# Performance work log

Hardware: AMD Instinct MI355X
Metric: run time of the kernel (lower is better)

## Reference

```python
import jax, jax.numpy as jnp
import numpy as np

N_CHR = 23
N_EMB = 512
E_DIM = 128
B = 4
L = 2048


def setup_inputs() -> dict:
    key = jax.random.key(0)
    k1, k2, k3 = jax.random.split(key, 3)
    chromosome = jax.random.randint(k1, (B, N_CHR, L), 0, N_CHR)
    position = jax.random.uniform(k2, (B, N_CHR, L), dtype=jnp.float32)
    embeddings = jax.random.normal(k3, (N_CHR, N_EMB, E_DIM), dtype=jnp.float32)
    centers = jnp.tile(jnp.linspace(0.0, 1.0, N_EMB, dtype=jnp.float32)[None, :], (N_CHR, 1))  # [23,512]
    log_variances = jnp.full((N_CHR, N_EMB), -5.0, dtype=jnp.float32)
    return {
        "chromosome": chromosome,
        "position": position,
        "embeddings": embeddings,
        "centers": centers,
        "log_variances": log_variances,
    }


def reference(chromosome, position, embeddings, centers, log_variances):
    # position: [B, C=23, L]; centers/log_variances: [C, K=512]; embeddings: [C, K, E]
    variances = jnp.exp(log_variances)                       # [C, K]
    d = position[..., None] - centers[None, :, None, :]      # [B, C, L, K]
    rbf = jnp.exp(-(d * d) / (2.0 * variances[None, :, None, :]))
    weights = jax.nn.softmax(rbf, axis=-1)                   # softmax over codebook (matches torch)
    out = jnp.einsum("bclk,cke->bcle", weights, embeddings)  # [B, C, L, E]
    bsz = position.shape[0]
    return out.reshape(bsz, -1, embeddings.shape[-1])        # [B, C*L, E]
```

## Files before the change

kernel.cpp:

```cpp
#include <hip/hip_runtime.h>
#include <hip/hip_bf16.h>

#define N_CHR 23
#define N_EMB 512
#define E_DIM 128
#define B_SZ  4
#define L_SEQ 2048
#define LOG2E 1.4426950408889634f
#define LOG2_LOG2E 0.5287663729448977f

typedef __attribute__((ext_vector_type(8))) short short8;
typedef __attribute__((ext_vector_type(4))) float floatx4;
typedef __attribute__((ext_vector_type(2))) float f32x2;

#if __has_builtin(__builtin_amdgcn_exp2f)
#define EXP2(x) __builtin_amdgcn_exp2f(x)
#else
#define EXP2(x) __expf((x) * 0.6931471805599453f)
#endif

#if __has_builtin(__builtin_amdgcn_rcpf)
#define RCP(x) __builtin_amdgcn_rcpf(x)
#else
#define RCP(x) (1.0f / (x))
#endif

__device__ __forceinline__ float bf2f(unsigned short u) {
    return __uint_as_float(((unsigned)u) << 16);
}
__device__ __forceinline__ unsigned short f2bf(float f) {
    unsigned u = __float_as_uint(f);
    unsigned r = u + 0x7FFFu + ((u >> 16) & 1u);
    return (unsigned short)(r >> 16);
}

__global__ __launch_bounds__(256) void emb_pack_kernel(
    const float* __restrict__ emb, uint4* __restrict__ embw)
{
    const int idx  = blockIdx.x * 256 + threadIdx.x;
    const int lane = idx & 63;
    const int nt   = (idx >> 6) & 7;
    const int ch   = (idx >> 9) & 15;
    const int c    = idx >> 13;
    if (c >= N_CHR) return;
    const int quad = lane >> 4;
    const int n    = nt * 16 + (lane & 15);
    const float* src = emb + (size_t)(c * N_EMB + ch * 32 + quad * 8) * E_DIM + n;
    unsigned v[8];
#pragma unroll
    for (int j = 0; j < 8; ++j) v[j] = (unsigned)f2bf(src[j * E_DIM]);
    uint4 w;
    w.x = v[0] | (v[1] << 16);
    w.y = v[2] | (v[3] << 16);
    w.z = v[4] | (v[5] << 16);
    w.w = v[6] | (v[7] << 16);
    embw[idx] = w;
}

__global__ __launch_bounds__(256, 7) void rbf_emb_kernel(
    const float* __restrict__ pos,
    const uint4* __restrict__ embw,
    const float* __restrict__ ctr,
    const float* __restrict__ lvar,
    float* __restrict__ out)
{
    __shared__ float2 cs_s[N_EMB];
    __shared__ uint4 Bs[2][512];

    const int tid  = threadIdx.x;
    const int lane = tid & 63;
    const int wave = tid >> 6;
    const int quad = lane >> 4;
    const int m    = lane & 15;

    const int bc   = blockIdx.x >> 5;
    const int mt   = blockIdx.x & 31;
    const int c    = bc % N_CHR;
    const int row0 = mt * 64;

    const uint4* gbase = embw + (size_t)c * (16 * 8 * 64);

    {
        const uint4* g = gbase + wave * 128 + lane;
        __builtin_amdgcn_global_load_lds(
            (const __attribute__((address_space(1))) void*)(g),
            (__attribute__((address_space(3))) void*)(&Bs[0][wave * 128]), 16, 0, 0);
        __builtin_amdgcn_global_load_lds(
            (const __attribute__((address_space(1))) void*)(g + 64),
            (__attribute__((address_space(3))) void*)(&Bs[0][wave * 128 + 64]), 16, 0, 0);
    }

    for (int k = tid; k < N_EMB; k += 256) {
        cs_s[k] = make_float2(ctr[c * N_EMB + k],
                              -0.5f * LOG2E * __expf(-lvar[c * N_EMB + k]));
    }

    const float posf = pos[bc * L_SEQ + row0 + wave * 16 + m];

    floatx4 acc[8];
#pragma unroll
    for (int i = 0; i < 8; ++i) acc[i] = (floatx4){0.f, 0.f, 0.f, 0.f};
    floatx4 accd = (floatx4){0.f, 0.f, 0.f, 0.f};

    short8 bones;
#pragma unroll
    for (int j = 0; j < 8; ++j) bones[j] = (short)0x3F80;

    auto computeA = [&](int ch) -> short8 {
        const float4* cs4 = ((const float4*)cs_s) + ch * 16 + quad * 4;
        unsigned pk[4];
#pragma unroll
        for (int jj = 0; jj < 4; ++jj) {
            const float4 q = cs4[jj];
            f32x2 cc = {q.x, q.z};
            f32x2 ss = {q.y, q.w};
            f32x2 d  = (f32x2){posf, posf} - cc;
            f32x2 t  = d * d;
            t = t * ss + (f32x2){LOG2_LOG2E, LOG2_LOG2E};
            const float p0 = EXP2(EXP2(t.x));
            const float p1 = EXP2(EXP2(t.y));
            union { __hip_bfloat162 h; unsigned u; } cv;
            cv.h = __float22bfloat162_rn(make_float2(p0, p1));
            pk[jj] = cv.u;
        }
        const int4 v = make_int4((int)pk[0], (int)pk[1], (int)pk[2], (int)pk[3]);
        return __builtin_bit_cast(short8, v);
    };

    __syncthreads();
    short8 aNext = computeA(0);

    for (int ch = 0; ch < 16; ++ch) {
        __syncthreads();

        if (ch < 15) {
            const uint4* g = gbase + (ch + 1) * 512 + wave * 128 + lane;
            uint4* bw = Bs[(ch + 1) & 1];
            __builtin_amdgcn_global_load_lds(
                (const __attribute__((address_space(1))) void*)(g),
                (__attribute__((address_space(3))) void*)(bw + wave * 128), 16, 0, 0);
            __builtin_amdgcn_global_load_lds(
                (const __attribute__((address_space(1))) void*)(g + 64),
                (__attribute__((address_space(3))) void*)(bw + wave * 128 + 64), 16, 0, 0);
        }

        const short8 a = aNext;
        const uint4* br = Bs[ch & 1];

        accd = __builtin_amdgcn_mfma_f32_16x16x32_bf16(a, bones, accd, 0, 0, 0);
#pragma unroll
        for (int nt = 0; nt < 8; ++nt) {
            short8 bfrag = *(const short8*)&br[(nt << 6) + lane];
            acc[nt] = __builtin_amdgcn_mfma_f32_16x16x32_bf16(a, bfrag, acc[nt], 0, 0, 0);
        }

        if (ch < 15) aNext = computeA(ch + 1);
    }

    float* outp = out + (size_t)(bc * L_SEQ + row0 + wave * 16) * E_DIM;
#pragma unroll
    for (int reg = 0; reg < 4; ++reg) {
        const float inv = RCP(accd[reg]);
        float* o = outp + (quad * 4 + reg) * E_DIM + m;
#pragma unroll
        for (int nt = 0; nt < 8; ++nt) {
            o[nt * 16] = acc[nt][reg] * inv;
        }
    }
}

__global__ __launch_bounds__(256, 4) void rbf_emb_kernel_slow(
    const float* __restrict__ pos, const float* __restrict__ emb,
    const float* __restrict__ ctr, const float* __restrict__ lvar,
    float* __restrict__ out)
{
    __shared__ float centers_s[N_EMB];
    __shared__ float scale_s[N_EMB];
    __shared__ uint4 Bs[2][512];
    __shared__ float inv_s[64];

    const int tid  = threadIdx.x;
    const int lane = tid & 63;
    const int wave = tid >> 6;
    const int quad = lane >> 4;
    const int m    = lane & 15;
    const int bc   = blockIdx.x >> 5;
    const int mt   = blockIdx.x & 31;
    const int c    = bc % N_CHR;
    const int row0 = mt * 64;

    for (int k = tid; k < N_EMB; k += 256) {
        centers_s[k] = ctr[c * N_EMB + k];
        scale_s[k]   = -0.5f * __expf(-lvar[c * N_EMB + k]);
    }
    const float posf = pos[bc * L_SEQ + row0 + wave * 16 + m];
    floatx4 acc[8];
#pragma unroll
    for (int i = 0; i < 8; ++i) acc[i] = (floatx4){0.f, 0.f, 0.f, 0.f};
    float denom = 0.f;
    __syncthreads();

    const int n_st = tid & 127;
    const int qd0  = tid >> 7;
    const float* embc = emb + (size_t)c * (N_EMB * E_DIM);

    for (int ch = 0; ch < 16; ++ch) {
        const int kc = ch * 32;
        uint4* bw = Bs[ch & 1];
#pragma unroll
        for (int qq = 0; qq < 2; ++qq) {
            const int qd = qd0 + qq * 2;
            const float* src = embc + (kc + qd * 8) * E_DIM + n_st;
            unsigned v[8];
#pragma unroll
            for (int j = 0; j < 8; ++j) v[j] = (unsigned)f2bf(src[j * E_DIM]);
            uint4 w;
            w.x = v[0] | (v[1] << 16);
            w.y = v[2] | (v[3] << 16);
            w.z = v[4] | (v[5] << 16);
            w.w = v[6] | (v[7] << 16);
            bw[((n_st >> 4) << 6) + (qd << 4) + (n_st & 15)] = w;
        }
        short8 afrag;
#pragma unroll
        for (int j = 0; j < 8; ++j) {
            const int   k   = kc + quad * 8 + j;
            const float d   = posf - centers_s[k];
            const float rbf = __expf(d * d * scale_s[k]);
            const float p   = __expf(rbf);
            const unsigned short pb = f2bf(p);
            afrag[j] = (short)pb;
            denom += bf2f(pb);
        }
        __syncthreads();
        const uint4* br = bw;
#pragma unroll
        for (int nt = 0; nt < 8; ++nt) {
            short8 bfrag = *(const short8*)&br[(nt << 6) + lane];
            acc[nt] = __builtin_amdgcn_mfma_f32_16x16x32_bf16(afrag, bfrag, acc[nt], 0, 0, 0);
        }
    }
    denom += __shfl_xor(denom, 16);
    denom += __shfl_xor(denom, 32);
    if (lane < 16) inv_s[wave * 16 + m] = 1.0f / denom;
    __syncthreads();
    float* outp = out + (size_t)(bc * L_SEQ + row0 + wave * 16) * E_DIM;
#pragma unroll
    for (int reg = 0; reg < 4; ++reg) {
        const int   r   = quad * 4 + reg;
        const float inv = inv_s[wave * 16 + r];
        float* o = outp + r * E_DIM + m;
#pragma unroll
        for (int nt = 0; nt < 8; ++nt) o[nt * 16] = acc[nt][reg] * inv;
    }
}

extern "C" void kernel_launch(void* const* d_in, const int* in_sizes, int n_in,
                              void* d_out, int out_size, void* d_ws, size_t ws_size,
                              hipStream_t stream) {
    const float* pos  = (const float*)d_in[1];
    const float* emb  = (const float*)d_in[2];
    const float* ctr  = (const float*)d_in[3];
    const float* lvar = (const float*)d_in[4];
    float* out = (float*)d_out;

    const int    blocks    = (B_SZ * N_CHR) * (L_SEQ / 64);
    const size_t ws_needed = (size_t)N_CHR * 16 * 8 * 64 * 16;

    if (ws_size >= ws_needed) {
        uint4* embw = (uint4*)d_ws;
        emb_pack_kernel<<<(N_CHR * 16 * 8 * 64) / 256, 256, 0, stream>>>(emb, embw);
        rbf_emb_kernel<<<blocks, 256, 0, stream>>>(pos, embw, ctr, lvar, out);
    } else {
        rbf_emb_kernel_slow<<<blocks, 256, 0, stream>>>(pos, emb, ctr, lvar, out);
    }
}
```

Baseline: 145.9 us.

## Process two 16-row M tiles per wave to reuse B fragments from LDS

Each wave now computes 32 rows instead of 16, so each block covers 128 rows and the grid is halved. Every B fragment read from LDS feeds two MFMAs, which halves LDS reads and the per-row cost of the embedding and centers staging. Launch bounds drop from 7 to 4 waves per SIMD to make room for the doubled accumulators, so occupancy and latency hiding fall, and the exp computation per chunk doubles per thread.

```diff
diff --git a/kernel.cpp b/kernel.cpp
--- a/kernel.cpp
+++ b/kernel.cpp
@@ -57,7 +57,7 @@
     embw[idx] = w;
 }
 
-__global__ __launch_bounds__(256, 7) void rbf_emb_kernel(
+__global__ __launch_bounds__(256, 4) void rbf_emb_kernel(
     const float* __restrict__ pos,
     const uint4* __restrict__ embw,
     const float* __restrict__ ctr,
@@ -73,10 +73,10 @@
     const int quad = lane >> 4;
     const int m    = lane & 15;
 
-    const int bc   = blockIdx.x >> 5;
-    const int mt   = blockIdx.x & 31;
+    const int bc   = blockIdx.x >> 4;
+    const int mt   = blockIdx.x & 15;
     const int c    = bc % N_CHR;
-    const int row0 = mt * 64;
+    const int row0 = mt * 128;
 
     const uint4* gbase = embw + (size_t)c * (16 * 8 * 64);
 
@@ -95,40 +95,52 @@
                               -0.5f * LOG2E * __expf(-lvar[c * N_EMB + k]));
     }
 
-    const float posf = pos[bc * L_SEQ + row0 + wave * 16 + m];
-
-    floatx4 acc[8];
-#pragma unroll
-    for (int i = 0; i < 8; ++i) acc[i] = (floatx4){0.f, 0.f, 0.f, 0.f};
-    floatx4 accd = (floatx4){0.f, 0.f, 0.f, 0.f};
+    const float posf0 = pos[bc * L_SEQ + row0 + wave * 32 + m];
+    const float posf1 = pos[bc * L_SEQ + row0 + wave * 32 + 16 + m];
+
+    floatx4 acc0[8], acc1[8];
+#pragma unroll
+    for (int i = 0; i < 8; ++i) {
+        acc0[i] = (floatx4){0.f, 0.f, 0.f, 0.f};
+        acc1[i] = (floatx4){0.f, 0.f, 0.f, 0.f};
+    }
+    floatx4 accd0 = (floatx4){0.f, 0.f, 0.f, 0.f};
+    floatx4 accd1 = (floatx4){0.f, 0.f, 0.f, 0.f};
 
     short8 bones;
 #pragma unroll
     for (int j = 0; j < 8; ++j) bones[j] = (short)0x3F80;
 
-    auto computeA = [&](int ch) -> short8 {
+    short8 aN0, aN1;
+    auto computeA2 = [&](int ch) {
         const float4* cs4 = ((const float4*)cs_s) + ch * 16 + quad * 4;
-        unsigned pk[4];
+        unsigned pk0[4], pk1[4];
 #pragma unroll
         for (int jj = 0; jj < 4; ++jj) {
             const float4 q = cs4[jj];
-            f32x2 cc = {q.x, q.z};
-            f32x2 ss = {q.y, q.w};
-            f32x2 d  = (f32x2){posf, posf} - cc;
-            f32x2 t  = d * d;
-            t = t * ss + (f32x2){LOG2_LOG2E, LOG2_LOG2E};
-            const float p0 = EXP2(EXP2(t.x));
-            const float p1 = EXP2(EXP2(t.y));
-            union { __hip_bfloat162 h; unsigned u; } cv;
-            cv.h = __float22bfloat162_rn(make_float2(p0, p1));
-            pk[jj] = cv.u;
-        }
-        const int4 v = make_int4((int)pk[0], (int)pk[1], (int)pk[2], (int)pk[3]);
-        return __builtin_bit_cast(short8, v);
+            const f32x2 cc = {q.x, q.z};
+            const f32x2 ss = {q.y, q.w};
+            const f32x2 C2 = {LOG2_LOG2E, LOG2_LOG2E};
+            f32x2 d0 = (f32x2){posf0, posf0} - cc;
+            f32x2 d1 = (f32x2){posf1, posf1} - cc;
+            f32x2 t0 = d0 * d0 * ss + C2;
+            f32x2 t1 = d1 * d1 * ss + C2;
+            const float p00 = EXP2(EXP2(t0.x));
+            const float p01 = EXP2(EXP2(t0.y));
+            const float p10 = EXP2(EXP2(t1.x));
+            const float p11 = EXP2(EXP2(t1.y));
+            union { __hip_bfloat162 h; unsigned u; } cv0, cv1;
+            cv0.h = __float22bfloat162_rn(make_float2(p00, p01));
+            cv1.h = __float22bfloat162_rn(make_float2(p10, p11));
+            pk0[jj] = cv0.u;
+            pk1[jj] = cv1.u;
+        }
+        aN0 = __builtin_bit_cast(short8, make_int4((int)pk0[0], (int)pk0[1], (int)pk0[2], (int)pk0[3]));
+        aN1 = __builtin_bit_cast(short8, make_int4((int)pk1[0], (int)pk1[1], (int)pk1[2], (int)pk1[3]));
     };
 
     __syncthreads();
-    short8 aNext = computeA(0);
+    computeA2(0);
 
     for (int ch = 0; ch < 16; ++ch) {
         __syncthreads();
@@ -144,27 +156,33 @@
                 (__attribute__((address_space(3))) void*)(bw + wave * 128 + 64), 16, 0, 0);
         }
 
-        const short8 a = aNext;
+        const short8 a0 = aN0, a1 = aN1;
         const uint4* br = Bs[ch & 1];
 
-        accd = __builtin_amdgcn_mfma_f32_16x16x32_bf16(a, bones, accd, 0, 0, 0);
+        accd0 = __builtin_amdgcn_mfma_f32_16x16x32_bf16(a0, bones, accd0, 0, 0, 0);
+        accd1 = __builtin_amdgcn_mfma_f32_16x16x32_bf16(a1, bones, accd1, 0, 0, 0);
 #pragma unroll
         for (int nt = 0; nt < 8; ++nt) {
             short8 bfrag = *(const short8*)&br[(nt << 6) + lane];
-            acc[nt] = __builtin_amdgcn_mfma_f32_16x16x32_bf16(a, bfrag, acc[nt], 0, 0, 0);
-        }
-
-        if (ch < 15) aNext = computeA(ch + 1);
-    }
-
-    float* outp = out + (size_t)(bc * L_SEQ + row0 + wave * 16) * E_DIM;
+            acc0[nt] = __builtin_amdgcn_mfma_f32_16x16x32_bf16(a0, bfrag, acc0[nt], 0, 0, 0);
+            acc1[nt] = __builtin_amdgcn_mfma_f32_16x16x32_bf16(a1, bfrag, acc1[nt], 0, 0, 0);
+        }
+
+        if (ch < 15) computeA2(ch + 1);
+    }
+
+    float* outp0 = out + (size_t)(bc * L_SEQ + row0 + wave * 32) * E_DIM;
+    float* outp1 = outp0 + 16 * E_DIM;
 #pragma unroll
     for (int reg = 0; reg < 4; ++reg) {
-        const float inv = RCP(accd[reg]);
-        float* o = outp + (quad * 4 + reg) * E_DIM + m;
+        const float inv0 = RCP(accd0[reg]);
+        const float inv1 = RCP(accd1[reg]);
+        float* o0 = outp0 + (quad * 4 + reg) * E_DIM + m;
+        float* o1 = outp1 + (quad * 4 + reg) * E_DIM + m;
 #pragma unroll
         for (int nt = 0; nt < 8; ++nt) {
-            o[nt * 16] = acc[nt][reg] * inv;
+            o0[nt * 16] = acc0[nt][reg] * inv0;
+            o1[nt * 16] = acc1[nt][reg] * inv1;
         }
     }
 }
@@ -264,14 +282,15 @@
     const float* lvar = (const float*)d_in[4];
     float* out = (float*)d_out;
 
-    const int    blocks    = (B_SZ * N_CHR) * (L_SEQ / 64);
     const size_t ws_needed = (size_t)N_CHR * 16 * 8 * 64 * 16;
 
     if (ws_size >= ws_needed) {
         uint4* embw = (uint4*)d_ws;
         emb_pack_kernel<<<(N_CHR * 16 * 8 * 64) / 256, 256, 0, stream>>>(emb, embw);
+        const int blocks = (B_SZ * N_CHR) * (L_SEQ / 128);
         rbf_emb_kernel<<<blocks, 256, 0, stream>>>(pos, embw, ctr, lvar, out);
     } else {
+        const int blocks = (B_SZ * N_CHR) * (L_SEQ / 64);
         rbf_emb_kernel_slow<<<blocks, 256, 0, stream>>>(pos, emb, ctr, lvar, out);
     }
 }
```

Result: no change. 143.8 us (-1.5%).
